# Performance work log

Hardware: AMD Instinct MI355X
Metric: run time of the kernel (lower is better)

## Reference

```python
import jax, jax.numpy as jnp
import numpy as np

D_MODEL = 1024
NUM_HEADS = 16
D_K = D_MODEL // NUM_HEADS
D_FF = 4096
B, S = 4, 2048
EPS = 1e-5


def _linear_params(key, d_in, d_out):
    # torch nn.Linear default init: U(-1/sqrt(d_in), 1/sqrt(d_in))
    k1, k2 = jax.random.split(key)
    bound = 1.0 / np.sqrt(d_in)
    W = jax.random.uniform(k1, (d_in, d_out), jnp.float32, -bound, bound)
    b = jax.random.uniform(k2, (d_out,), jnp.float32, -bound, bound)
    return W, b


def setup_inputs() -> dict:
    key = jax.random.key(0)
    ks = jax.random.split(key, 8)
    x = jax.random.normal(ks[0], (B, S, D_MODEL), jnp.float32)
    Wq, bq = _linear_params(ks[1], D_MODEL, D_MODEL)
    Wk, bk = _linear_params(ks[2], D_MODEL, D_MODEL)
    Wv, bv = _linear_params(ks[3], D_MODEL, D_MODEL)
    Wo, bo = _linear_params(ks[4], D_MODEL, D_MODEL)
    W1, b1 = _linear_params(ks[5], D_MODEL, D_FF)
    W2, b2 = _linear_params(ks[6], D_FF, D_MODEL)
    ln1_g = jnp.ones((D_MODEL,), jnp.float32)
    ln1_b = jnp.zeros((D_MODEL,), jnp.float32)
    ln2_g = jnp.ones((D_MODEL,), jnp.float32)
    ln2_b = jnp.zeros((D_MODEL,), jnp.float32)
    return dict(x=x, Wq=Wq, bq=bq, Wk=Wk, bk=bk, Wv=Wv, bv=bv, Wo=Wo, bo=bo,
                W1=W1, b1=b1, W2=W2, b2=b2,
                ln1_g=ln1_g, ln1_b=ln1_b, ln2_g=ln2_g, ln2_b=ln2_b)


def _layernorm(x, g, b):
    mu = jnp.mean(x, axis=-1, keepdims=True)
    var = jnp.mean(jnp.square(x - mu), axis=-1, keepdims=True)
    return (x - mu) * jax.lax.rsqrt(var + EPS) * g + b


def _attention(h, Wq, bq, Wk, bk, Wv, bv, Wo, bo):
    b, s, _ = h.shape
    def split_heads(t):  # (b,s,d) -> (b,H,s,dk)
        return t.reshape(b, s, NUM_HEADS, D_K).transpose(0, 2, 1, 3)
    Q = split_heads(h @ Wq + bq)
    K = split_heads(h @ Wk + bk)
    V = split_heads(h @ Wv + bv)
    scores = jnp.einsum('bhqd,bhkd->bhqk', Q, K) / np.sqrt(D_K)
    causal = jnp.tril(jnp.ones((s, s), dtype=bool))  # True = keep
    scores = jnp.where(causal, scores, -jnp.inf)
    attn = jax.nn.softmax(scores, axis=-1)
    out = jnp.einsum('bhqk,bhkd->bhqd', attn, V)
    out = out.transpose(0, 2, 1, 3).reshape(b, s, D_MODEL)
    return out @ Wo + bo


def reference(x, Wq, bq, Wk, bk, Wv, bv, Wo, bo, W1, b1, W2, b2,
              ln1_g, ln1_b, ln2_g, ln2_b):
    # pre-norm residual block
    x = x + _attention(_layernorm(x, ln1_g, ln1_b), Wq, bq, Wk, bk, Wv, bv, Wo, bo)
    h = _layernorm(x, ln2_g, ln2_b)
    x = x + (jax.nn.relu(h @ W1 + b1) @ W2 + b2)
    return x
```

## Files before the change

### kernel.cpp

```cpp
#include <hip/hip_runtime.h>
#include <hip/hip_bf16.h>

typedef __bf16 bf16;
typedef __attribute__((ext_vector_type(8))) __bf16 bf16x8;
typedef __attribute__((ext_vector_type(4))) float f32x4;

#define D_MODEL 1024
#define NHEADS  16
#define DK      64
#define DFF     4096
#define BATCH   4
#define SEQ     2048
#define NTOK    (BATCH*SEQ)
#define QSCALE  0.18033688011112042f

__device__ __forceinline__ void gload16(const bf16* g, bf16* l) {
    __builtin_amdgcn_global_load_lds((const __attribute__((address_space(1))) void*)g,
                                     (__attribute__((address_space(3))) void*)l, 16, 0, 0);
}

__global__ __launch_bounds__(256) void transpose_cast4(
    const float* __restrict__ W0, const float* __restrict__ W1,
    const float* __restrict__ W2, const float* __restrict__ W3,
    bf16* __restrict__ T0, bf16* __restrict__ T1,
    bf16* __restrict__ T2, bf16* __restrict__ T3)
{
    const int z = blockIdx.z;
    const float* W = (z == 0) ? W0 : (z == 1) ? W1 : (z == 2) ? W2 : W3;
    bf16*       Wt = (z == 0) ? T0 : (z == 1) ? T1 : (z == 2) ? T2 : T3;
    const int K = 1024, N = 1024;
    __shared__ float tile[32][33];
    const int tx = threadIdx.x, ty = threadIdx.y;
    const int n0 = blockIdx.x * 32, k0 = blockIdx.y * 32;
#pragma unroll
    for (int i = 0; i < 4; ++i)
        tile[ty + i*8][tx] = W[(size_t)(k0 + ty + i*8) * N + n0 + tx];
    __syncthreads();
#pragma unroll
    for (int i = 0; i < 4; ++i)
        Wt[(size_t)(n0 + ty + i*8) * K + k0 + tx] = (bf16)tile[tx][ty + i*8];
}

__global__ __launch_bounds__(256) void transpose_cast(
    const float* __restrict__ W, bf16* __restrict__ Wt, int K, int N)
{
    __shared__ float tile[32][33];
    const int tx = threadIdx.x, ty = threadIdx.y;
    const int n0 = blockIdx.x * 32, k0 = blockIdx.y * 32;
#pragma unroll
    for (int i = 0; i < 4; ++i)
        tile[ty + i*8][tx] = W[(size_t)(k0 + ty + i*8) * N + n0 + tx];
    __syncthreads();
#pragma unroll
    for (int i = 0; i < 4; ++i)
        Wt[(size_t)(n0 + ty + i*8) * K + k0 + tx] = (bf16)tile[tx][ty + i*8];
}

__global__ __launch_bounds__(256) void transpose_v(
    const bf16* __restrict__ V, bf16* __restrict__ VT)
{
    __shared__ bf16 t[64][72];
    const int bh = blockIdx.y;
    const int s0 = blockIdx.x * 64;
    const int r  = threadIdx.x >> 2;
    const int c0 = (threadIdx.x & 3) * 16;
    const bf16* Vb = V  + (size_t)bh * SEQ * DK;
    bf16*       Tb = VT + (size_t)bh * DK * SEQ;
#pragma unroll
    for (int i = 0; i < 2; ++i) {
        bf16x8 v = *(const bf16x8*)&Vb[(size_t)(s0 + r) * DK + c0 + i*8];
#pragma unroll
        for (int j = 0; j < 8; ++j) t[c0 + i*8 + j][r] = v[j];
    }
    __syncthreads();
#pragma unroll
    for (int i = 0; i < 2; ++i) {
        bf16x8 o;
#pragma unroll
        for (int j = 0; j < 8; ++j) o[j] = t[r][c0 + i*8 + j];
        *(bf16x8*)&Tb[(size_t)r * SEQ + s0 + c0 + i*8] = o;
    }
}

__global__ __launch_bounds__(256) void ln_kernel(
    const float* __restrict__ x, const float* __restrict__ g,
    const float* __restrict__ beta, bf16* __restrict__ out)
{
    const int row = blockIdx.x, tid = threadIdx.x;
    const f32x4* xr = (const f32x4*)(x + (size_t)row * D_MODEL);
    f32x4 v = xr[tid];
    float s  = v[0] + v[1] + v[2] + v[3];
    float s2 = v[0]*v[0] + v[1]*v[1] + v[2]*v[2] + v[3]*v[3];
#pragma unroll
    for (int off = 32; off > 0; off >>= 1) {
        s  += __shfl_down(s,  off, 64);
        s2 += __shfl_down(s2, off, 64);
    }
    __shared__ float red[8];
    const int wave = tid >> 6, lane = tid & 63;
    if (lane == 0) { red[wave] = s; red[wave + 4] = s2; }
    __syncthreads();
    if (tid == 0) {
        float a = red[0] + red[1] + red[2] + red[3];
        float c = red[4] + red[5] + red[6] + red[7];
        float mu  = a * (1.0f / D_MODEL);
        float var = c * (1.0f / D_MODEL) - mu * mu;
        red[0] = mu;
        red[1] = rsqrtf(var + 1e-5f);
    }
    __syncthreads();
    const float mu = red[0], rs = red[1];
    f32x4 gv = ((const f32x4*)g)[tid];
    f32x4 bv = ((const f32x4*)beta)[tid];
    union { bf16 h[4]; uint2 u; } o;
#pragma unroll
    for (int i = 0; i < 4; ++i) o.h[i] = (bf16)((v[i] - mu) * rs * gv[i] + bv[i]);
    *(uint2*)(out + (size_t)row * D_MODEL + tid * 4) = o.u;
}

template<int EPI>
__global__ __launch_bounds__(256, 2) void gemm_bf16(
    const bf16* __restrict__ A, const bf16* __restrict__ Bt,
    const float* __restrict__ bias, const float* __restrict__ bias2,
    const float* __restrict__ bias3, const float* __restrict__ resid,
    void* __restrict__ outp, int M, int N, int K)
{
    __shared__ __align__(16) bf16 As[128 * 32];
    __shared__ __align__(16) bf16 Bs[128 * 32];
    const int tid  = threadIdx.x;
    const int wave = tid >> 6, lane = tid & 63;
    const int quad = lane >> 4, l16 = lane & 15;
    const int wr = wave >> 1, wc = wave & 1;
    const int m0 = blockIdx.x * 128, n0 = blockIdx.y * 128;

    const int r0 = wave * 32 + (lane >> 2);
    const int r1 = r0 + 16;
    const int u0 = ((lane & 3) - ((r0 >> 1) & 3)) & 3;
    const int u1 = ((lane & 3) - ((r1 >> 1) & 3)) & 3;
    const bf16* gA0 = A  + (size_t)(m0 + r0) * K + u0 * 8;
    const bf16* gA1 = A  + (size_t)(m0 + r1) * K + u1 * 8;
    const bf16* gB0 = Bt + (size_t)(n0 + r0) * K + u0 * 8;
    const bf16* gB1 = Bt + (size_t)(n0 + r1) * K + u1 * 8;
    bf16* lA0 = As + wave * 1024;
    bf16* lA1 = As + wave * 1024 + 512;
    bf16* lB0 = Bs + wave * 1024;
    bf16* lB1 = Bs + wave * 1024 + 512;

    int aoff[4], boff[4];
#pragma unroll
    for (int i = 0; i < 4; ++i) {
        const int ra = wr * 64 + i * 16 + l16;
        aoff[i] = ra * 32 + ((quad + ((ra >> 1) & 3)) & 3) * 8;
        const int rb = wc * 64 + i * 16 + l16;
        boff[i] = rb * 32 + ((quad + ((rb >> 1) & 3)) & 3) * 8;
    }

    const f32x4 vzero = {0.f, 0.f, 0.f, 0.f};
    f32x4 acc[4][4];
#pragma unroll
    for (int i = 0; i < 4; ++i)
#pragma unroll
        for (int j = 0; j < 4; ++j) acc[i][j] = vzero;

    for (int k0 = 0; k0 < K; k0 += 32) {
        __syncthreads();
        gload16(gA0 + k0, lA0);
        gload16(gA1 + k0, lA1);
        gload16(gB0 + k0, lB0);
        gload16(gB1 + k0, lB1);
        __syncthreads();
        bf16x8 af[4], bfr[4];
#pragma unroll
        for (int i = 0; i < 4; ++i) af[i]  = *(const bf16x8*)&As[aoff[i]];
#pragma unroll
        for (int j = 0; j < 4; ++j) bfr[j] = *(const bf16x8*)&Bs[boff[j]];
#pragma unroll
        for (int i = 0; i < 4; ++i)
#pragma unroll
            for (int j = 0; j < 4; ++j)
                acc[i][j] = __builtin_amdgcn_mfma_f32_16x16x32_bf16(af[i], bfr[j], acc[i][j], 0, 0, 0);
    }

#pragma unroll
    for (int i = 0; i < 4; ++i) {
#pragma unroll
        for (int j = 0; j < 4; ++j) {
            const int col = n0 + wc * 64 + j * 16 + l16;
            float bcol, sc = 1.0f;
            if (EPI == 0) {
                const int seg = col >> 10;
                const float* bp = (seg == 0) ? bias : ((seg == 1) ? bias2 : bias3);
                bcol = bp[col & 1023];
                if (seg == 0) sc = QSCALE;
            } else {
                bcol = bias[col];
            }
#pragma unroll
            for (int r = 0; r < 4; ++r) {
                const int row = m0 + wr * 64 + i * 16 + quad * 4 + r;
                const float v = acc[i][j][r] + bcol;
                if (EPI == 0) {
                    const int bb = row >> 11, ss = row & (SEQ - 1);
                    const int hh = (col & 1023) >> 6, dd = col & (DK - 1);
                    const size_t seg = (size_t)(col >> 10);
                    ((bf16*)outp)[seg * 8388608 + (((size_t)(bb * NHEADS + hh)) * SEQ + ss) * DK + dd] = (bf16)(v * sc);
                } else if (EPI == 1) {
                    const size_t idx = (size_t)row * N + col;
                    ((float*)outp)[idx] = v + resid[idx];
                } else {
                    ((bf16*)outp)[(size_t)row * N + col] = (bf16)fmaxf(v, 0.f);
                }
            }
        }
    }
}

__global__ __launch_bounds__(256, 2) void attn_kernel(
    const bf16* __restrict__ Q, const bf16* __restrict__ K,
    const bf16* __restrict__ VT, bf16* __restrict__ out)
{
    const int bh = blockIdx.x;
    const int b = bh >> 4, h = bh & 15;
    const int tid  = threadIdx.x;
    const int wave = tid >> 6, lane = tid & 63;
    const int quad = lane >> 4, l16 = lane & 15;

    __shared__ __align__(16) bf16 smem[32768 + 4 * 1152];
    bf16* Pw = smem + 32768 + wave * 1152;

    const bf16* Qb = Q  + (size_t)bh * SEQ * DK;
    const bf16* Kb = K  + (size_t)bh * SEQ * DK;
    const bf16* Vb = VT + (size_t)bh * DK * SEQ;

    int goK[4], goV[4], lo[4];
#pragma unroll
    for (int i = 0; i < 4; ++i) {
        const int U = (wave * 4 + i) * 64 + lane;
        const int rK = U >> 3, uK = (U & 7) ^ (rK & 7);
        goK[i] = rK * DK + uK * 8;
        const int rV = U >> 4, usw = U & 15;
        const int uV = (usw & 8) | ((usw & 7) ^ (rV & 7));
        goV[i] = rV * SEQ + uV * 8;
        lo[i]  = (wave * 4 + i) * 512;
    }

    auto stage = [&](int buf, int t) {
        const bf16* kp = Kb + (size_t)(t * 128) * DK;
        const bf16* vp = Vb + t * 128;
        bf16* kb = smem + buf * 8192;
        bf16* vb = smem + 16384 + buf * 8192;
#pragma unroll
        for (int i = 0; i < 4; ++i) gload16(kp + goK[i], kb + lo[i]);
#pragma unroll
        for (int i = 0; i < 4; ++i) gload16(vp + goV[i], vb + lo[i]);
    };

    const f32x4 vzero = {0.f, 0.f, 0.f, 0.f};
    int g = 0;
    stage(0, 0);

    for (int phase = 0; phase < 2; ++phase) {
        const int qt = phase ? (int)blockIdx.y : 15 - (int)blockIdx.y;
        const int qw = qt * 128 + wave * 32;

        bf16x8 qf[2][2];
#pragma unroll
        for (int qi = 0; qi < 2; ++qi)
#pragma unroll
            for (int kk = 0; kk < 2; ++kk)
                qf[qi][kk] = *(const bf16x8*)&Qb[(size_t)(qw + qi*16 + l16) * DK + kk*32 + quad*8];

        f32x4 Oacc[2][4];
        float m_[2], l_[2];
#pragma unroll
        for (int qi = 0; qi < 2; ++qi) {
            m_[qi] = -1.0e30f; l_[qi] = 0.f;
#pragma unroll
            for (int dj = 0; dj < 4; ++dj) Oacc[qi][dj] = vzero;
        }

        for (int t = 0; t <= qt; ++t, ++g) {
            const int cur = g & 1;
            __syncthreads();
            if (t < qt)            stage(cur ^ 1, t + 1);
            else if (phase == 0)   stage(cur ^ 1, 0);
            const bf16* kb = smem + cur * 8192;
            const bf16* vb = smem + 16384 + cur * 8192;
            const int kv0 = t * 128;

            f32x4 sv[8][2];
#pragma unroll
            for (int kvt = 0; kvt < 8; ++kvt) {
                const int R = kvt*16 + l16, rx = R & 7;
                bf16x8 kf0 = *(const bf16x8*)&kb[R*64 + (quad ^ rx)*8];
                bf16x8 kf1 = *(const bf16x8*)&kb[R*64 + (((quad + 4) & 7) ^ rx)*8];
#pragma unroll
                for (int qi = 0; qi < 2; ++qi) {
                    f32x4 tacc = vzero;
                    tacc = __builtin_amdgcn_mfma_f32_16x16x32_bf16(kf0, qf[qi][0], tacc, 0, 0, 0);
                    tacc = __builtin_amdgcn_mfma_f32_16x16x32_bf16(kf1, qf[qi][1], tacc, 0, 0, 0);
                    sv[kvt][qi] = tacc;
                }
            }

            if (t == qt) {
#pragma unroll
                for (int kvt = 0; kvt < 8; ++kvt)
#pragma unroll
                    for (int qi = 0; qi < 2; ++qi)
#pragma unroll
                        for (int r = 0; r < 4; ++r) {
                            const int kv = kv0 + kvt*16 + quad*4 + r;
                            const int q  = qw + qi*16 + l16;
                            if (kv > q) sv[kvt][qi][r] = -1.0e30f;
                        }
            }

#pragma unroll
            for (int qi = 0; qi < 2; ++qi) {
                float mx = sv[0][qi][0];
#pragma unroll
                for (int kvt = 0; kvt < 8; ++kvt)
#pragma unroll
                    for (int r = 0; r < 4; ++r) mx = fmaxf(mx, sv[kvt][qi][r]);
                mx = fmaxf(mx, __shfl_xor(mx, 16, 64));
                mx = fmaxf(mx, __shfl_xor(mx, 32, 64));
                const float newm  = fmaxf(m_[qi], mx);
                const float alpha = exp2f(m_[qi] - newm);
                m_[qi] = newm;
                float rs = 0.f;
#pragma unroll
                for (int kvt = 0; kvt < 8; ++kvt)
#pragma unroll
                    for (int r = 0; r < 4; ++r) {
                        const float p = exp2f(sv[kvt][qi][r] - newm);
                        sv[kvt][qi][r] = p;
                        rs += p;
                    }
                rs += __shfl_xor(rs, 16, 64);
                rs += __shfl_xor(rs, 32, 64);
                l_[qi] = l_[qi] * alpha + rs;
#pragma unroll
                for (int dj = 0; dj < 4; ++dj) Oacc[qi][dj] *= alpha;
            }

#pragma unroll
            for (int c2 = 0; c2 < 4; ++c2) {
#pragma unroll
                for (int qi = 0; qi < 2; ++qi)
#pragma unroll
                    for (int kl = 0; kl < 2; ++kl) {
                        union { bf16 h[4]; unsigned long long u; } pk;
                        const f32x4 s = sv[c2*2 + kl][qi];
#pragma unroll
                        for (int r = 0; r < 4; ++r) pk.h[r] = (bf16)s[r];
                        *(unsigned long long*)&Pw[(qi*16 + l16)*36 + kl*16 + quad*4] = pk.u;
                    }
                bf16x8 vf[4];
#pragma unroll
                for (int dj = 0; dj < 4; ++dj) {
                    const int R = dj*16 + l16;
                    const int u = c2*4 + quad;
                    const int usw = (u & 8) | ((u & 7) ^ (R & 7));
                    vf[dj] = *(const bf16x8*)&vb[R*128 + usw*8];
                }
#pragma unroll
                for (int qi = 0; qi < 2; ++qi) {
                    bf16x8 pf = *(const bf16x8*)&Pw[(qi*16 + l16)*36 + quad*8];
#pragma unroll
                    for (int dj = 0; dj < 4; ++dj)
                        Oacc[qi][dj] = __builtin_amdgcn_mfma_f32_16x16x32_bf16(vf[dj], pf, Oacc[qi][dj], 0, 0, 0);
                }
            }
        }

        const float inv0 = 1.0f / l_[0], inv1 = 1.0f / l_[1];
#pragma unroll
        for (int dh = 0; dh < 2; ++dh) {
#pragma unroll
            for (int qi = 0; qi < 2; ++qi) {
                const float inv = qi ? inv1 : inv0;
#pragma unroll
                for (int djl = 0; djl < 2; ++djl) {
                    const int dj = dh*2 + djl;
                    union { bf16 h[4]; unsigned long long u; } ok;
#pragma unroll
                    for (int r = 0; r < 4; ++r) ok.h[r] = (bf16)(Oacc[qi][dj][r] * inv);
                    *(unsigned long long*)&Pw[(qi*16 + l16)*36 + djl*16 + quad*4] = ok.u;
                }
            }
            const int row = lane >> 1;
#pragma unroll
            for (int it = 0; it < 2; ++it) {
                const int grp = (lane & 1) + 2*it;
                bf16x8 o = *(const bf16x8*)&Pw[row*36 + grp*8];
                *(bf16x8*)&out[((size_t)(b*SEQ + qw - wave*32 + wave*32 + row))*D_MODEL + h*DK + dh*32 + grp*8] = o;
            }
        }
    }
}

extern "C" void kernel_launch(void* const* d_in, const int* in_sizes, int n_in,
                              void* d_out, int out_size, void* d_ws, size_t ws_size,
                              hipStream_t stream)
{
    const float* x    = (const float*)d_in[0];
    const float* Wq   = (const float*)d_in[1];
    const float* bq   = (const float*)d_in[2];
    const float* Wk   = (const float*)d_in[3];
    const float* bk   = (const float*)d_in[4];
    const float* Wv   = (const float*)d_in[5];
    const float* bv   = (const float*)d_in[6];
    const float* Wo   = (const float*)d_in[7];
    const float* bo   = (const float*)d_in[8];
    const float* W1   = (const float*)d_in[9];
    const float* b1   = (const float*)d_in[10];
    const float* W2   = (const float*)d_in[11];
    const float* b2   = (const float*)d_in[12];
    const float* ln1g = (const float*)d_in[13];
    const float* ln1b = (const float*)d_in[14];
    const float* ln2g = (const float*)d_in[15];
    const float* ln2b = (const float*)d_in[16];

    char* ws = (char*)d_ws;
    const size_t MB = 1024 * 1024;
    bf16* WTq  = (bf16*)(ws + 0 * MB);
    bf16* WTk  = (bf16*)(ws + 2 * MB);
    bf16* WTv  = (bf16*)(ws + 4 * MB);
    bf16* WTo  = (bf16*)(ws + 6 * MB);
    bf16* WT1  = (bf16*)(ws + 8 * MB);
    bf16* WT2  = (bf16*)(ws + 16 * MB);
    bf16* hbuf = (bf16*)(ws + 24 * MB);
    bf16* VhT  = (bf16*)(ws + 24 * MB);
    bf16* Qh   = (bf16*)(ws + 40 * MB);
    bf16* Kh   = (bf16*)(ws + 56 * MB);
    bf16* Vh   = (bf16*)(ws + 72 * MB);
    bf16* attn = (bf16*)(ws + 88 * MB);
    bf16* ff1  = (bf16*)(ws + 40 * MB);
    float* x2  = (float*)d_out;

    dim3 tb(32, 8);
    transpose_cast4<<<dim3(32, 32, 4), tb, 0, stream>>>(Wq, Wk, Wv, Wo, WTq, WTk, WTv, WTo);
    transpose_cast<<<dim3(128, 32), tb, 0, stream>>>(W1, WT1, 1024, 4096);
    transpose_cast<<<dim3(32, 128), tb, 0, stream>>>(W2, WT2, 4096, 1024);

    ln_kernel<<<NTOK, 256, 0, stream>>>(x, ln1g, ln1b, hbuf);

    gemm_bf16<0><<<dim3(64, 24), 256, 0, stream>>>(hbuf, WTq, bq, bk, bv, nullptr, Qh, NTOK, 3072, 1024);

    transpose_v<<<dim3(32, 64), 256, 0, stream>>>(Vh, VhT);

    attn_kernel<<<dim3(64, 8), 256, 0, stream>>>(Qh, Kh, VhT, attn);

    gemm_bf16<1><<<dim3(64, 8), 256, 0, stream>>>(attn, WTo, bo, nullptr, nullptr, x, x2, NTOK, 1024, 1024);

    ln_kernel<<<NTOK, 256, 0, stream>>>(x2, ln2g, ln2b, hbuf);

    gemm_bf16<2><<<dim3(64, 32), 256, 0, stream>>>(hbuf, WT1, b1, nullptr, nullptr, nullptr, ff1, NTOK, 4096, 1024);
    gemm_bf16<1><<<dim3(64, 8),  256, 0, stream>>>(ff1, WT2, b2, nullptr, nullptr, x2, x2, NTOK, 1024, 4096);
}
```

Before: 519.2 us.

## Split attention across 8 waves and use 128x64 tiles for N=1024 GEMMs

The attention kernel now runs 512 threads per block, with each wave owning 16 query rows instead of 32, which halves per-wave registers and increases wave-level parallelism. The out-projection and FFN2 GEMMs move to a new kernel with a 128x64 tile and a residual-add epilogue, doubling the block count to fill more CUs. The new GEMM uses a simple synchronous load loop with two barriers per k-step, which may expose memory latency. Each attention wave also performs less MFMA work per K/V tile load, so LDS reads of K and V are amortized over fewer rows.

Result: slower. 533.0 us (+2.7%).

```diff
diff --git a/kernel.cpp b/kernel.cpp
--- a/kernel.cpp
+++ b/kernel.cpp
@@ -122,7 +122,7 @@
 __global__ __launch_bounds__(256, 2) void gemm_bf16(
     const bf16* __restrict__ A, const bf16* __restrict__ Bt,
     const float* __restrict__ bias, const float* __restrict__ bias2,
-    const float* __restrict__ bias3, const float* __restrict__ resid,
+    const float* __restrict__ bias3,
     void* __restrict__ outp, int M, int N, int K)
 {
     __shared__ __align__(16) bf16 As[128 * 32];
@@ -204,9 +204,6 @@
                     const int hh = (col & 1023) >> 6, dd = col & (DK - 1);
                     const size_t seg = (size_t)(col >> 10);
                     ((bf16*)outp)[seg * 8388608 + (((size_t)(bb * NHEADS + hh)) * SEQ + ss) * DK + dd] = (bf16)(v * sc);
-                } else if (EPI == 1) {
-                    const size_t idx = (size_t)row * N + col;
-                    ((float*)outp)[idx] = v + resid[idx];
                 } else {
                     ((bf16*)outp)[(size_t)row * N + col] = (bf16)fmaxf(v, 0.f);
                 }
@@ -215,7 +212,85 @@
     }
 }
 
-__global__ __launch_bounds__(256, 2) void attn_kernel(
+__global__ __launch_bounds__(256, 4) void gemm_n64(
+    const bf16* __restrict__ A, const bf16* __restrict__ Bt,
+    const float* __restrict__ bias, const float* __restrict__ resid,
+    float* __restrict__ outp, int M, int N, int K)
+{
+    __shared__ __align__(16) bf16 As[128 * 32];
+    __shared__ __align__(16) bf16 Bs[64 * 32];
+    const int tid  = threadIdx.x;
+    const int wave = tid >> 6, lane = tid & 63;
+    const int quad = lane >> 4, l16 = lane & 15;
+    const int m0 = blockIdx.x * 128, n0 = blockIdx.y * 64;
+
+    const int r0 = wave * 32 + (lane >> 2);
+    const int r1 = r0 + 16;
+    const int u0 = ((lane & 3) - ((r0 >> 1) & 3)) & 3;
+    const int u1 = ((lane & 3) - ((r1 >> 1) & 3)) & 3;
+    const bf16* gA0 = A + (size_t)(m0 + r0) * K + u0 * 8;
+    const bf16* gA1 = A + (size_t)(m0 + r1) * K + u1 * 8;
+    bf16* lA0 = As + wave * 1024;
+    bf16* lA1 = As + wave * 1024 + 512;
+    const int rb = wave * 16 + (lane >> 2);
+    const int ub = ((lane & 3) - ((rb >> 1) & 3)) & 3;
+    const bf16* gB = Bt + (size_t)(n0 + rb) * K + ub * 8;
+    bf16* lB = Bs + wave * 512;
+
+    int aoff[2], boff[4];
+#pragma unroll
+    for (int i = 0; i < 2; ++i) {
+        const int ra = wave * 32 + i * 16 + l16;
+        aoff[i] = ra * 32 + ((quad + ((ra >> 1) & 3)) & 3) * 8;
+    }
+#pragma unroll
+    for (int j = 0; j < 4; ++j) {
+        const int rbn = j * 16 + l16;
+        boff[j] = rbn * 32 + ((quad + ((rbn >> 1) & 3)) & 3) * 8;
+    }
+
+    const f32x4 vzero = {0.f, 0.f, 0.f, 0.f};
+    f32x4 acc[2][4];
+#pragma unroll
+    for (int i = 0; i < 2; ++i)
+#pragma unroll
+        for (int j = 0; j < 4; ++j) acc[i][j] = vzero;
+
+    for (int k0 = 0; k0 < K; k0 += 32) {
+        __syncthreads();
+        gload16(gA0 + k0, lA0);
+        gload16(gA1 + k0, lA1);
+        gload16(gB  + k0, lB);
+        __syncthreads();
+        bf16x8 af[2], bfr[4];
+#pragma unroll
+        for (int i = 0; i < 2; ++i) af[i]  = *(const bf16x8*)&As[aoff[i]];
+#pragma unroll
+        for (int j = 0; j < 4; ++j) bfr[j] = *(const bf16x8*)&Bs[boff[j]];
+#pragma unroll
+        for (int i = 0; i < 2; ++i)
+#pragma unroll
+            for (int j = 0; j < 4; ++j)
+                acc[i][j] = __builtin_amdgcn_mfma_f32_16x16x32_bf16(af[i], bfr[j], acc[i][j], 0, 0, 0);
+    }
+
+#pragma unroll
+    for (int i = 0; i < 2; ++i) {
+#pragma unroll
+        for (int j = 0; j < 4; ++j) {
+            const int col = n0 + j * 16 + l16;
+            const float bcol = bias[col];
+#pragma unroll
+            for (int r = 0; r < 4; ++r) {
+                const int row = m0 + wave * 32 + i * 16 + quad * 4 + r;
+                const size_t idx = (size_t)row * N + col;
+                outp[idx] = acc[i][j][r] + bcol + resid[idx];
+            }
+        }
+    }
+}
+
+__global__ __launch_bounds__(512, 4) void attn_kernel(
     const bf16* __restrict__ Q, const bf16* __restrict__ K,
     const bf16* __restrict__ VT, bf16* __restrict__ out)
 {
@@ -225,23 +300,23 @@
     const int wave = tid >> 6, lane = tid & 63;
     const int quad = lane >> 4, l16 = lane & 15;
 
-    __shared__ __align__(16) bf16 smem[32768 + 4 * 1152];
-    bf16* Pw = smem + 32768 + wave * 1152;
+    __shared__ __align__(16) bf16 smem[32768 + 8 * 576];
+    bf16* Pw = smem + 32768 + wave * 576;
 
     const bf16* Qb = Q  + (size_t)bh * SEQ * DK;
     const bf16* Kb = K  + (size_t)bh * SEQ * DK;
     const bf16* Vb = VT + (size_t)bh * DK * SEQ;
 
-    int goK[4], goV[4], lo[4];
-#pragma unroll
-    for (int i = 0; i < 4; ++i) {
-        const int U = (wave * 4 + i) * 64 + lane;
+    int goK[2], goV[2], lo[2];
+#pragma unroll
+    for (int i = 0; i < 2; ++i) {
+        const int U = (wave * 2 + i) * 64 + lane;
         const int rK = U >> 3, uK = (U & 7) ^ (rK & 7);
         goK[i] = rK * DK + uK * 8;
         const int rV = U >> 4, usw = U & 15;
         const int uV = (usw & 8) | ((usw & 7) ^ (rV & 7));
         goV[i] = rV * SEQ + uV * 8;
-        lo[i]  = (wave * 4 + i) * 512;
+        lo[i]  = (wave * 2 + i) * 512;
     }
 
     auto stage = [&](int buf, int t) {
@@ -250,9 +325,9 @@
         bf16* kb = smem + buf * 8192;
         bf16* vb = smem + 16384 + buf * 8192;
 #pragma unroll
-        for (int i = 0; i < 4; ++i) gload16(kp + goK[i], kb + lo[i]);
-#pragma unroll
-        for (int i = 0; i < 4; ++i) gload16(vp + goV[i], vb + lo[i]);
+        for (int i = 0; i < 2; ++i) gload16(kp + goK[i], kb + lo[i]);
+#pragma unroll
+        for (int i = 0; i < 2; ++i) gload16(vp + goV[i], vb + lo[i]);
     };
 
     const f32x4 vzero = {0.f, 0.f, 0.f, 0.f};
@@ -261,23 +336,17 @@
 
     for (int phase = 0; phase < 2; ++phase) {
         const int qt = phase ? (int)blockIdx.y : 15 - (int)blockIdx.y;
-        const int qw = qt * 128 + wave * 32;
-
-        bf16x8 qf[2][2];
-#pragma unroll
-        for (int qi = 0; qi < 2; ++qi)
-#pragma unroll
-            for (int kk = 0; kk < 2; ++kk)
-                qf[qi][kk] = *(const bf16x8*)&Qb[(size_t)(qw + qi*16 + l16) * DK + kk*32 + quad*8];
-
-        f32x4 Oacc[2][4];
-        float m_[2], l_[2];
-#pragma unroll
-        for (int qi = 0; qi < 2; ++qi) {
-            m_[qi] = -1.0e30f; l_[qi] = 0.f;
-#pragma unroll
-            for (int dj = 0; dj < 4; ++dj) Oacc[qi][dj] = vzero;
-        }
+        const int qw = qt * 128 + wave * 16;
+
+        bf16x8 qf[2];
+#pragma unroll
+        for (int kk = 0; kk < 2; ++kk)
+            qf[kk] = *(const bf16x8*)&Qb[(size_t)(qw + l16) * DK + kk*32 + quad*8];
+
+        f32x4 Oacc[4];
+        float m_ = -1.0e30f, l_ = 0.f;
+#pragma unroll
+        for (int dj = 0; dj < 4; ++dj) Oacc[dj] = vzero;
 
         for (int t = 0; t <= qt; ++t, ++g) {
             const int cur = g & 1;
@@ -288,74 +357,66 @@
             const bf16* vb = smem + 16384 + cur * 8192;
             const int kv0 = t * 128;
 
-            f32x4 sv[8][2];
+            f32x4 sv[8];
 #pragma unroll
             for (int kvt = 0; kvt < 8; ++kvt) {
                 const int R = kvt*16 + l16, rx = R & 7;
                 bf16x8 kf0 = *(const bf16x8*)&kb[R*64 + (quad ^ rx)*8];
                 bf16x8 kf1 = *(const bf16x8*)&kb[R*64 + (((quad + 4) & 7) ^ rx)*8];
-#pragma unroll
-                for (int qi = 0; qi < 2; ++qi) {
-                    f32x4 tacc = vzero;
-                    tacc = __builtin_amdgcn_mfma_f32_16x16x32_bf16(kf0, qf[qi][0], tacc, 0, 0, 0);
-                    tacc = __builtin_amdgcn_mfma_f32_16x16x32_bf16(kf1, qf[qi][1], tacc, 0, 0, 0);
-                    sv[kvt][qi] = tacc;
-                }
+                f32x4 tacc = vzero;
+                tacc = __builtin_amdgcn_mfma_f32_16x16x32_bf16(kf0, qf[0], tacc, 0, 0, 0);
+                tacc = __builtin_amdgcn_mfma_f32_16x16x32_bf16(kf1, qf[1], tacc, 0, 0, 0);
+                sv[kvt] = tacc;
             }
 
             if (t == qt) {
 #pragma unroll
                 for (int kvt = 0; kvt < 8; ++kvt)
 #pragma unroll
-                    for (int qi = 0; qi < 2; ++qi)
-#pragma unroll
-                        for (int r = 0; r < 4; ++r) {
-                            const int kv = kv0 + kvt*16 + quad*4 + r;
-                            const int q  = qw + qi*16 + l16;
-                            if (kv > q) sv[kvt][qi][r] = -1.0e30f;
-                        }
-            }
-
-#pragma unroll
-            for (int qi = 0; qi < 2; ++qi) {
-                float mx = sv[0][qi][0];
+                    for (int r = 0; r < 4; ++r) {
+                        const int kv = kv0 + kvt*16 + quad*4 + r;
+                        const int q  = qw + l16;
+                        if (kv > q) sv[kvt][r] = -1.0e30f;
+                    }
+            }
+
+            {
+                float mx = sv[0][0];
 #pragma unroll
                 for (int kvt = 0; kvt < 8; ++kvt)
 #pragma unroll
-                    for (int r = 0; r < 4; ++r) mx = fmaxf(mx, sv[kvt][qi][r]);
+                    for (int r = 0; r < 4; ++r) mx = fmaxf(mx, sv[kvt][r]);
                 mx = fmaxf(mx, __shfl_xor(mx, 16, 64));
                 mx = fmaxf(mx, __shfl_xor(mx, 32, 64));
-                const float newm  = fmaxf(m_[qi], mx);
-                const float alpha = exp2f(m_[qi] - newm);
-                m_[qi] = newm;
+                const float newm  = fmaxf(m_, mx);
+                const float alpha = exp2f(m_ - newm);
+                m_ = newm;
                 float rs = 0.f;
 #pragma unroll
                 for (int kvt = 0; kvt < 8; ++kvt)
 #pragma unroll
                     for (int r = 0; r < 4; ++r) {
-                        const float p = exp2f(sv[kvt][qi][r] - newm);
-                        sv[kvt][qi][r] = p;
+                        const float p = exp2f(sv[kvt][r] - newm);
+                        sv[kvt][r] = p;
                         rs += p;
                     }
                 rs += __shfl_xor(rs, 16, 64);
                 rs += __shfl_xor(rs, 32, 64);
-                l_[qi] = l_[qi] * alpha + rs;
-#pragma unroll
-                for (int dj = 0; dj < 4; ++dj) Oacc[qi][dj] *= alpha;
+                l_ = l_ * alpha + rs;
+#pragma unroll
+                for (int dj = 0; dj < 4; ++dj) Oacc[dj] *= alpha;
             }
 
 #pragma unroll
             for (int c2 = 0; c2 < 4; ++c2) {
 #pragma unroll
-                for (int qi = 0; qi < 2; ++qi)
-#pragma unroll
-                    for (int kl = 0; kl < 2; ++kl) {
-                        union { bf16 h[4]; unsigned long long u; } pk;
-                        const f32x4 s = sv[c2*2 + kl][qi];
-#pragma unroll
-                        for (int r = 0; r < 4; ++r) pk.h[r] = (bf16)s[r];
-                        *(unsigned long long*)&Pw[(qi*16 + l16)*36 + kl*16 + quad*4] = pk.u;
-                    }
+                for (int kl = 0; kl < 2; ++kl) {
+                    union { bf16 h[4]; unsigned long long u; } pk;
+                    const f32x4 s = sv[c2*2 + kl];
+#pragma unroll
+                    for (int r = 0; r < 4; ++r) pk.h[r] = (bf16)s[r];
+                    *(unsigned long long*)&Pw[l16*36 + kl*16 + quad*4] = pk.u;
+                }
                 bf16x8 vf[4];
 #pragma unroll
                 for (int dj = 0; dj < 4; ++dj) {
@@ -364,38 +425,27 @@
                     const int usw = (u & 8) | ((u & 7) ^ (R & 7));
                     vf[dj] = *(const bf16x8*)&vb[R*128 + usw*8];
                 }
-#pragma unroll
-                for (int qi = 0; qi < 2; ++qi) {
-                    bf16x8 pf = *(const bf16x8*)&Pw[(qi*16 + l16)*36 + quad*8];
-#pragma unroll
-                    for (int dj = 0; dj < 4; ++dj)
-                        Oacc[qi][dj] = __builtin_amdgcn_mfma_f32_16x16x32_bf16(vf[dj], pf, Oacc[qi][dj], 0, 0, 0);
-                }
+                bf16x8 pf = *(const bf16x8*)&Pw[l16*36 + quad*8];
+#pragma unroll
+                for (int dj = 0; dj < 4; ++dj)
+                    Oacc[dj] = __builtin_amdgcn_mfma_f32_16x16x32_bf16(vf[dj], pf, Oacc[dj], 0, 0, 0);
             }
         }
 
-        const float inv0 = 1.0f / l_[0], inv1 = 1.0f / l_[1];
+        const float inv = 1.0f / l_;
 #pragma unroll
         for (int dh = 0; dh < 2; ++dh) {
 #pragma unroll
-            for (int qi = 0; qi < 2; ++qi) {
-                const float inv = qi ? inv1 : inv0;
-#pragma unroll
-                for (int djl = 0; djl < 2; ++djl) {
-                    const int dj = dh*2 + djl;
-                    union { bf16 h[4]; unsigned long long u; } ok;
-#pragma unroll
-                    for (int r = 0; r < 4; ++r) ok.h[r] = (bf16)(Oacc[qi][dj][r] * inv);
-                    *(unsigned long long*)&Pw[(qi*16 + l16)*36 + djl*16 + quad*4] = ok.u;
-                }
-            }
-            const int row = lane >> 1;
-#pragma unroll
-            for (int it = 0; it < 2; ++it) {
-                const int grp = (lane & 1) + 2*it;
-                bf16x8 o = *(const bf16x8*)&Pw[row*36 + grp*8];
-                *(bf16x8*)&out[((size_t)(b*SEQ + qw - wave*32 + wave*32 + row))*D_MODEL + h*DK + dh*32 + grp*8] = o;
-            }
+            for (int djl = 0; djl < 2; ++djl) {
+                const int dj = dh*2 + djl;
+                union { bf16 h[4]; unsigned long long u; } ok;
+#pragma unroll
+                for (int r = 0; r < 4; ++r) ok.h[r] = (bf16)(Oacc[dj][r] * inv);
+                *(unsigned long long*)&Pw[l16*36 + djl*16 + quad*4] = ok.u;
+            }
+            const int row = lane >> 2, grp = lane & 3;
+            bf16x8 o = *(const bf16x8*)&Pw[row*36 + grp*8];
+            *(bf16x8*)&out[((size_t)(b*SEQ + qw - wave*16 + wave*16 + row))*D_MODEL + h*DK + dh*32 + grp*8] = o;
         }
     }
 }
@@ -446,16 +496,16 @@
 
     ln_kernel<<<NTOK, 256, 0, stream>>>(x, ln1g, ln1b, hbuf);
 
-    gemm_bf16<0><<<dim3(64, 24), 256, 0, stream>>>(hbuf, WTq, bq, bk, bv, nullptr, Qh, NTOK, 3072, 1024);
+    gemm_bf16<0><<<dim3(64, 24), 256, 0, stream>>>(hbuf, WTq, bq, bk, bv, Qh, NTOK, 3072, 1024);
 
     transpose_v<<<dim3(32, 64), 256, 0, stream>>>(Vh, VhT);
 
-    attn_kernel<<<dim3(64, 8), 256, 0, stream>>>(Qh, Kh, VhT, attn);
-
-    gemm_bf16<1><<<dim3(64, 8), 256, 0, stream>>>(attn, WTo, bo, nullptr, nullptr, x, x2, NTOK, 1024, 1024);
+    attn_kernel<<<dim3(64, 8), 512, 0, stream>>>(Qh, Kh, VhT, attn);
+
+    gemm_n64<<<dim3(64, 16), 256, 0, stream>>>(attn, WTo, bo, x, x2, NTOK, 1024, 1024);
 
     ln_kernel<<<NTOK, 256, 0, stream>>>(x2, ln2g, ln2b, hbuf);
 
-    gemm_bf16<2><<<dim3(64, 32), 256, 0, stream>>>(hbuf, WT1, b1, nullptr, nullptr, nullptr, ff1, NTOK, 4096, 1024);
-    gemm_bf16<1><<<dim3(64, 8),  256, 0, stream>>>(ff1, WT2, b2, nullptr, nullptr, x2, x2, NTOK, 1024, 4096);
-}
+    gemm_bf16<2><<<dim3(64, 32), 256, 0, stream>>>(hbuf, WT1, b1, nullptr, nullptr, ff1, NTOK, 4096, 1024);
+    gemm_n64<<<dim3(64, 16), 256, 0, stream>>>(ff1, WT2, b2, x2, x2, NTOK, 1024, 4096);
+}
```
